# Optimization experiments

Measured on AMD Instinct MI355X. Metric: run time of the kernel, lower is better.

Reference implementation:

```python
import jax, jax.numpy as jnp
import numpy as np


def setup_inputs() -> dict:
    key = jax.random.key(0)
    ks = jax.random.split(key, 10)
    N1, N2, F, D, E = 50000, 50000, 1024, 128, 1000000
    s = 0.02
    return {
        "x_gene": jax.random.normal(ks[0], (N1, F), jnp.float32),
        "x_cell": jax.random.normal(ks[1], (N2, F), jnp.float32),
        "edge_label_index": jax.random.randint(ks[2], (2, E), 0, N1, jnp.int64 if jax.config.jax_enable_x64 else jnp.int32),
        "W1": jax.random.normal(ks[3], (F, D), jnp.float32) * s,
        "b1": jnp.zeros((D,), jnp.float32),
        "W2": jax.random.normal(ks[4], (F, D), jnp.float32) * s,
        "b2": jnp.zeros((D,), jnp.float32),
        "Wm1": jax.random.normal(ks[5], (2 * D, 64), jnp.float32) * s,
        "bm1": jnp.zeros((64,), jnp.float32),
        "Wm2": jax.random.normal(ks[6], (64, 32), jnp.float32) * s,
        "bm2": jnp.zeros((32,), jnp.float32),
        "Wm3": jax.random.normal(ks[7], (32, 1), jnp.float32) * s,
        "bm3": jnp.zeros((1,), jnp.float32),
    }


def reference(x_gene, x_cell, edge_label_index, W1, b1, W2, b2, Wm1, bm1, Wm2, bm2, Wm3, bm3):
    # Node-type linear projections (dropout is identity in eval mode)
    h1 = x_gene @ W1 + b1          # [N1, D]
    h2 = x_cell @ W2 + b2          # [N2, D]
    # Edge gather + concat
    ef = jnp.concatenate([h1[edge_label_index[0]], h2[edge_label_index[1]]], axis=-1)  # [E, 2D]
    # 3-layer MLP classifier
    h = jax.nn.relu(ef @ Wm1 + bm1)
    h = jax.nn.relu(h @ Wm2 + bm2)
    pred = (h @ Wm3 + bm3)[..., 0]  # squeeze(-1) -> [E]
    return pred
```

## Files before the change

### kernel.cpp

```cpp
#include <hip/hip_runtime.h>
#include <hip/hip_bf16.h>
#include <stdint.h>

typedef __attribute__((ext_vector_type(8))) short short8;
typedef __attribute__((ext_vector_type(4))) float float4v;

__device__ __forceinline__ float bf2f(uint16_t u) {
    union { uint32_t i; float f; } v; v.i = ((uint32_t)u) << 16; return v.f;
}
__device__ __forceinline__ uint16_t f2bf(float f) {
    union { float f; uint32_t i; } v; v.f = f;
    uint32_t x = v.i;
    uint32_t r = (x + 0x7fffu + ((x >> 16) & 1u)) >> 16;
    return (uint16_t)r;
}
__device__ __forceinline__ float relu_nanprop(float x) {
    return 0.5f * (x + fabsf(x));
}

__global__ __launch_bounds__(256) void precompute_kernel(
    const float* __restrict__ W1, const float* __restrict__ W2,
    const float* __restrict__ Wm1,
    const float* __restrict__ b1, const float* __restrict__ b2,
    const float* __restrict__ bm1,
    uint16_t* __restrict__ A1T, uint16_t* __restrict__ A2T,
    float* __restrict__ tbias)
{
    int b = blockIdx.x, t = threadIdx.x;
    if (b < 512) {
        int g   = b * 256 + t;
        int mat = g >> 16;
        int rem = g & 65535;
        int n   = rem >> 10;
        int f   = rem & 1023;
        const float* W  = mat ? W2 : W1;
        const float* wm = Wm1 + mat * 128 * 64;
        const float4* Wrow = (const float4*)(W + (size_t)f * 128);
        float acc = 0.f;
        #pragma unroll
        for (int c = 0; c < 32; ++c) {
            float4 w = Wrow[c];
            acc += w.x * wm[(c * 4 + 0) * 64 + n];
            acc += w.y * wm[(c * 4 + 1) * 64 + n];
            acc += w.z * wm[(c * 4 + 2) * 64 + n];
            acc += w.w * wm[(c * 4 + 3) * 64 + n];
        }
        (mat ? A2T : A1T)[(size_t)n * 1024 + f] = f2bf(acc);
    } else if (t < 64) {
        float acc = bm1[t];
        for (int d = 0; d < 128; ++d) acc += b1[d] * Wm1[d * 64 + t];
        for (int d = 0; d < 128; ++d) acc += b2[d] * Wm1[(128 + d) * 64 + t];
        tbias[t] = acc;
    }
}

__global__ __launch_bounds__(256) void gemm64_kernel(
    const float* __restrict__ X1, const float* __restrict__ X2,
    const uint16_t* __restrict__ A1T, const uint16_t* __restrict__ A2T,
    uint16_t* __restrict__ G1, uint16_t* __restrict__ G2, int M1, int M2)
{
    const int which = blockIdx.y;
    const float* __restrict__ X     = which ? X2  : X1;
    const uint16_t* __restrict__ BT = which ? A2T : A1T;
    uint16_t* __restrict__ G        = which ? G2  : G1;
    const int M = which ? M2 : M1;

    const int blockRow = blockIdx.x * 128;
    if (blockRow >= M) return;

    __shared__ uint16_t As[128 * 64];

    const int t    = threadIdx.x;
    const int wid  = t >> 6;
    const int lane = t & 63;
    const int m    = lane & 15;
    const int q    = lane >> 4;

    float4v acc[2][4];
    #pragma unroll
    for (int r = 0; r < 2; ++r)
        #pragma unroll
        for (int nt = 0; nt < 4; ++nt)
            acc[r][nt] = (float4v){0.f, 0.f, 0.f, 0.f};

    for (int kk = 0; kk < 16; ++kk) {
        float4 av0[4], av1[4];
        int    dstc[4];
        #pragma unroll
        for (int it = 0; it < 4; ++it) {
            int c   = it * 256 + t;
            int row = c >> 3, pc = c & 7;
            int lc  = pc ^ (row & 7);
            int grow = blockRow + row; if (grow >= M) grow = M - 1;
            const float4* src = (const float4*)(X + (size_t)grow * 1024 + kk * 64 + lc * 8);
            av0[it] = src[0];
            av1[it] = src[1];
            dstc[it] = c * 8;
        }
        __syncthreads();
        #pragma unroll
        for (int it = 0; it < 4; ++it) {
            uint4 pk;
            pk.x = (uint32_t)f2bf(av0[it].x) | ((uint32_t)f2bf(av0[it].y) << 16);
            pk.y = (uint32_t)f2bf(av0[it].z) | ((uint32_t)f2bf(av0[it].w) << 16);
            pk.z = (uint32_t)f2bf(av1[it].x) | ((uint32_t)f2bf(av1[it].y) << 16);
            pk.w = (uint32_t)f2bf(av1[it].z) | ((uint32_t)f2bf(av1[it].w) << 16);
            *(uint4*)(As + dstc[it]) = pk;
        }
        __syncthreads();

        #pragma unroll
        for (int s = 0; s < 2; ++s) {
            short8 af[2], bfr[4];
            #pragma unroll
            for (int r = 0; r < 2; ++r) {
                int row = wid * 32 + r * 16 + m;
                int pc  = (s * 4 + q) ^ (row & 7);
                af[r] = *(const short8*)(As + row * 64 + pc * 8);
            }
            #pragma unroll
            for (int nt = 0; nt < 4; ++nt) {
                int n = nt * 16 + m;
                bfr[nt] = *(const short8*)(BT + (size_t)n * 1024 + kk * 64 + (s * 4 + q) * 8);
            }
            #pragma unroll
            for (int r = 0; r < 2; ++r)
                #pragma unroll
                for (int nt = 0; nt < 4; ++nt)
                    acc[r][nt] = __builtin_amdgcn_mfma_f32_16x16x32_bf16(
                        af[r], bfr[nt], acc[r][nt], 0, 0, 0);
        }
    }

    #pragma unroll
    for (int r = 0; r < 2; ++r) {
        #pragma unroll
        for (int reg = 0; reg < 4; ++reg) {
            int grow = blockRow + wid * 32 + r * 16 + q * 4 + reg;
            if (grow < M) {
                #pragma unroll
                for (int nt = 0; nt < 4; ++nt)
                    G[(size_t)grow * 64 + nt * 16 + m] = f2bf(acc[r][nt][reg]);
            }
        }
    }
}

__global__ __launch_bounds__(256) void edge_mlp_kernel(
    const uint16_t* __restrict__ g1, const uint16_t* __restrict__ g2,
    const float* __restrict__ tbias, const int* __restrict__ eidx,
    const float* __restrict__ Wm2, const float* __restrict__ bm2,
    const float* __restrict__ Wm3, const float* __restrict__ bm3,
    float* __restrict__ out, int E)
{
    int e = blockIdx.x * 256 + threadIdx.x;
    if (e >= E) e = E - 1;
    int src = eidx[e];
    int dst = eidx[E + e];
    const uint4* r1 = (const uint4*)(g1 + (size_t)src * 64);
    const uint4* r2 = (const uint4*)(g2 + (size_t)dst * 64);

    float u[32];
    #pragma unroll
    for (int j = 0; j < 32; ++j) u[j] = bm2[j];

    #pragma unroll
    for (int c = 0; c < 8; ++c) {
        uint4 a = r1[c], b = r2[c];
        uint32_t aw[4] = { a.x, a.y, a.z, a.w };
        uint32_t bw[4] = { b.x, b.y, b.z, b.w };
        float tv[8];
        #pragma unroll
        for (int h = 0; h < 4; ++h) {
            float alo, ahi, blo, bhi;
            { union { uint32_t i; float f; } v; v.i = aw[h] << 16;        alo = v.f; }
            { union { uint32_t i; float f; } v; v.i = aw[h] & 0xffff0000u; ahi = v.f; }
            { union { uint32_t i; float f; } v; v.i = bw[h] << 16;        blo = v.f; }
            { union { uint32_t i; float f; } v; v.i = bw[h] & 0xffff0000u; bhi = v.f; }
            tv[2 * h]     = relu_nanprop(alo + blo + tbias[c * 8 + 2 * h]);
            tv[2 * h + 1] = relu_nanprop(ahi + bhi + tbias[c * 8 + 2 * h + 1]);
        }
        #pragma unroll
        for (int i = 0; i < 8; ++i) {
            const float* wrow = Wm2 + (c * 8 + i) * 32;
            #pragma unroll
            for (int j = 0; j < 32; ++j)
                u[j] = fmaf(tv[i], wrow[j], u[j]);
        }
    }

    float p = bm3[0];
    #pragma unroll
    for (int j = 0; j < 32; ++j)
        p += relu_nanprop(u[j]) * Wm3[j];
    out[e] = p;
}

extern "C" void kernel_launch(void* const* d_in, const int* in_sizes, int n_in,
                              void* d_out, int out_size, void* d_ws, size_t ws_size,
                              hipStream_t stream) {
    const float* x_gene = (const float*)d_in[0];
    const float* x_cell = (const float*)d_in[1];
    const int*   eidx   = (const int*)d_in[2];
    const float* W1  = (const float*)d_in[3];
    const float* b1  = (const float*)d_in[4];
    const float* W2  = (const float*)d_in[5];
    const float* b2  = (const float*)d_in[6];
    const float* Wm1 = (const float*)d_in[7];
    const float* bm1 = (const float*)d_in[8];
    const float* Wm2 = (const float*)d_in[9];
    const float* bm2 = (const float*)d_in[10];
    const float* Wm3 = (const float*)d_in[11];
    const float* bm3 = (const float*)d_in[12];

    const int M1 = in_sizes[0] / 1024;
    const int M2 = in_sizes[1] / 1024;
    const int E  = in_sizes[2] / 2;

    uint8_t* ws = (uint8_t*)d_ws;
    uint16_t* A1T   = (uint16_t*)(ws + 0);
    uint16_t* A2T   = (uint16_t*)(ws + 131072);
    float*    tbias = (float*)(ws + 262144);
    uint16_t* G1    = (uint16_t*)(ws + 524288);
    size_t g1_bytes = ((size_t)M1 * 64 * 2 + 127) & ~(size_t)127;
    uint16_t* G2    = (uint16_t*)(ws + 524288 + g1_bytes);

    precompute_kernel<<<513, 256, 0, stream>>>(
        W1, W2, Wm1, b1, b2, bm1, A1T, A2T, tbias);

    int Mmax = M1 > M2 ? M1 : M2;
    dim3 ggrid((Mmax + 127) / 128, 2);
    gemm64_kernel<<<ggrid, 256, 0, stream>>>(x_gene, x_cell, A1T, A2T, G1, G2, M1, M2);

    edge_mlp_kernel<<<(E + 255) / 256, 256, 0, stream>>>(
        G1, G2, tbias, eidx, Wm2, bm2, Wm3, bm3, (float*)d_out, E);
}
```

Before: 573.7 us.

## Use MFMA for edge MLP layer 2, retile GEMM, and restructure precompute

The edge MLP now writes the relu'd hidden layer as bf16 into shared memory and computes the 64x32 second layer with bf16 MFMA, then finishes layer 3 with a cross-lane shuffle reduction instead of 2048 scalar FMAs per thread. The projection GEMM moves to 64-row blocks with 128-wide K steps, doubling the grid for more parallelism. The precompute kernel is reorganised to give coalesced weight reads, and it also emits a transposed bf16 copy of Wm2. This lowers ALU work in the edge stage, at the cost of bf16 rounding of the hidden activations and extra shared memory use.

```diff
diff --git a/kernel.cpp b/kernel.cpp
--- a/kernel.cpp
+++ b/kernel.cpp
@@ -14,43 +14,41 @@
     uint32_t r = (x + 0x7fffu + ((x >> 16) & 1u)) >> 16;
     return (uint16_t)r;
 }
-__device__ __forceinline__ float relu_nanprop(float x) {
-    return 0.5f * (x + fabsf(x));
-}
 
 __global__ __launch_bounds__(256) void precompute_kernel(
     const float* __restrict__ W1, const float* __restrict__ W2,
-    const float* __restrict__ Wm1,
+    const float* __restrict__ Wm1, const float* __restrict__ Wm2,
     const float* __restrict__ b1, const float* __restrict__ b2,
     const float* __restrict__ bm1,
     uint16_t* __restrict__ A1T, uint16_t* __restrict__ A2T,
-    float* __restrict__ tbias)
+    float* __restrict__ tbias, uint16_t* __restrict__ Wm2bfT)
 {
     int b = blockIdx.x, t = threadIdx.x;
     if (b < 512) {
-        int g   = b * 256 + t;
-        int mat = g >> 16;
-        int rem = g & 65535;
-        int n   = rem >> 10;
-        int f   = rem & 1023;
-        const float* W  = mat ? W2 : W1;
-        const float* wm = Wm1 + mat * 128 * 64;
-        const float4* Wrow = (const float4*)(W + (size_t)f * 128);
+        int g   = b * 4 + (t >> 6);
+        int mat = g >> 10;
+        int f   = g & 1023;
+        int n   = t & 63;
+        const float* W    = mat ? W2 : W1;
+        const float* wm   = Wm1 + mat * 128 * 64;
+        const float* Wrow = W + (size_t)f * 128;
         float acc = 0.f;
-        #pragma unroll
-        for (int c = 0; c < 32; ++c) {
-            float4 w = Wrow[c];
-            acc += w.x * wm[(c * 4 + 0) * 64 + n];
-            acc += w.y * wm[(c * 4 + 1) * 64 + n];
-            acc += w.z * wm[(c * 4 + 2) * 64 + n];
-            acc += w.w * wm[(c * 4 + 3) * 64 + n];
-        }
+        #pragma unroll 8
+        for (int d = 0; d < 128; ++d)
+            acc = fmaf(Wrow[d], wm[d * 64 + n], acc);
         (mat ? A2T : A1T)[(size_t)n * 1024 + f] = f2bf(acc);
-    } else if (t < 64) {
-        float acc = bm1[t];
-        for (int d = 0; d < 128; ++d) acc += b1[d] * Wm1[d * 64 + t];
-        for (int d = 0; d < 128; ++d) acc += b2[d] * Wm1[(128 + d) * 64 + t];
-        tbias[t] = acc;
+    } else {
+        int n  = t >> 3;
+        int k0 = (t & 7) * 8;
+        #pragma unroll
+        for (int i = 0; i < 8; ++i)
+            Wm2bfT[n * 64 + k0 + i] = f2bf(Wm2[(size_t)(k0 + i) * 32 + n]);
+        if (t < 64) {
+            float acc = bm1[t];
+            for (int d = 0; d < 128; ++d) acc += b1[d] * Wm1[d * 64 + t];
+            for (int d = 0; d < 128; ++d) acc += b2[d] * Wm1[(128 + d) * 64 + t];
+            tbias[t] = acc;
+        }
     }
 }
 
@@ -65,10 +63,10 @@
     uint16_t* __restrict__ G        = which ? G2  : G1;
     const int M = which ? M2 : M1;
 
-    const int blockRow = blockIdx.x * 128;
+    const int blockRow = blockIdx.x * 64;
     if (blockRow >= M) return;
 
-    __shared__ uint16_t As[128 * 64];
+    __shared__ uint16_t As[64 * 128];
 
     const int t    = threadIdx.x;
     const int wid  = t >> 6;
@@ -76,23 +74,20 @@
     const int m    = lane & 15;
     const int q    = lane >> 4;
 
-    float4v acc[2][4];
-    #pragma unroll
-    for (int r = 0; r < 2; ++r)
-        #pragma unroll
-        for (int nt = 0; nt < 4; ++nt)
-            acc[r][nt] = (float4v){0.f, 0.f, 0.f, 0.f};
-
-    for (int kk = 0; kk < 16; ++kk) {
+    float4v acc[4];
+    #pragma unroll
+    for (int nt = 0; nt < 4; ++nt) acc[nt] = (float4v){0.f, 0.f, 0.f, 0.f};
+
+    for (int kk = 0; kk < 8; ++kk) {
         float4 av0[4], av1[4];
         int    dstc[4];
         #pragma unroll
         for (int it = 0; it < 4; ++it) {
             int c   = it * 256 + t;
-            int row = c >> 3, pc = c & 7;
+            int row = c >> 4, pc = c & 15;
             int lc  = pc ^ (row & 7);
             int grow = blockRow + row; if (grow >= M) grow = M - 1;
-            const float4* src = (const float4*)(X + (size_t)grow * 1024 + kk * 64 + lc * 8);
+            const float4* src = (const float4*)(X + (size_t)grow * 1024 + kk * 128 + lc * 8);
             av0[it] = src[0];
             av1[it] = src[1];
             dstc[it] = c * 8;
@@ -110,38 +105,30 @@
         __syncthreads();
 
         #pragma unroll
-        for (int s = 0; s < 2; ++s) {
-            short8 af[2], bfr[4];
-            #pragma unroll
-            for (int r = 0; r < 2; ++r) {
-                int row = wid * 32 + r * 16 + m;
-                int pc  = (s * 4 + q) ^ (row & 7);
-                af[r] = *(const short8*)(As + row * 64 + pc * 8);
-            }
+        for (int p = 0; p < 4; ++p) {
+            short8 af, bfr[4];
+            int row = wid * 16 + m;
+            int pc  = (p * 4 + q) ^ (row & 7);
+            af = *(const short8*)(As + row * 128 + pc * 8);
             #pragma unroll
             for (int nt = 0; nt < 4; ++nt) {
                 int n = nt * 16 + m;
-                bfr[nt] = *(const short8*)(BT + (size_t)n * 1024 + kk * 64 + (s * 4 + q) * 8);
+                bfr[nt] = *(const short8*)(BT + (size_t)n * 1024 + kk * 128 + (p * 4 + q) * 8);
             }
             #pragma unroll
-            for (int r = 0; r < 2; ++r)
-                #pragma unroll
-                for (int nt = 0; nt < 4; ++nt)
-                    acc[r][nt] = __builtin_amdgcn_mfma_f32_16x16x32_bf16(
-                        af[r], bfr[nt], acc[r][nt], 0, 0, 0);
-        }
-    }
-
-    #pragma unroll
-    for (int r = 0; r < 2; ++r) {
-        #pragma unroll
-        for (int reg = 0; reg < 4; ++reg) {
-            int grow = blockRow + wid * 32 + r * 16 + q * 4 + reg;
-            if (grow < M) {
-                #pragma unroll
-                for (int nt = 0; nt < 4; ++nt)
-                    G[(size_t)grow * 64 + nt * 16 + m] = f2bf(acc[r][nt][reg]);
-            }
+            for (int nt = 0; nt < 4; ++nt)
+                acc[nt] = __builtin_amdgcn_mfma_f32_16x16x32_bf16(
+                    af, bfr[nt], acc[nt], 0, 0, 0);
+        }
+    }
+
+    #pragma unroll
+    for (int reg = 0; reg < 4; ++reg) {
+        int grow = blockRow + wid * 16 + q * 4 + reg;
+        if (grow < M) {
+            #pragma unroll
+            for (int nt = 0; nt < 4; ++nt)
+                G[(size_t)grow * 64 + nt * 16 + m] = f2bf(acc[nt][reg]);
         }
     }
 }
@@ -149,27 +136,45 @@
 __global__ __launch_bounds__(256) void edge_mlp_kernel(
     const uint16_t* __restrict__ g1, const uint16_t* __restrict__ g2,
     const float* __restrict__ tbias, const int* __restrict__ eidx,
-    const float* __restrict__ Wm2, const float* __restrict__ bm2,
+    const uint16_t* __restrict__ Wm2bfT, const float* __restrict__ bm2,
     const float* __restrict__ Wm3, const float* __restrict__ bm3,
     float* __restrict__ out, int E)
 {
-    int e = blockIdx.x * 256 + threadIdx.x;
-    if (e >= E) e = E - 1;
-    int src = eidx[e];
-    int dst = eidx[E + e];
+    __shared__ uint16_t T[256 * 64];
+
+    const int t    = threadIdx.x;
+    const int wid  = t >> 6;
+    const int lane = t & 63;
+    const int m    = lane & 15;
+    const int q    = lane >> 4;
+
+    short8 bfrag[2][2];
+    #pragma unroll
+    for (int s = 0; s < 2; ++s)
+        #pragma unroll
+        for (int nt = 0; nt < 2; ++nt)
+            bfrag[s][nt] = *(const short8*)(Wm2bfT + (nt * 16 + m) * 64 + s * 32 + q * 8);
+
+    const float bm2a = bm2[m],      bm2b = bm2[16 + m];
+    const float w3a  = Wm3[m],      w3b  = Wm3[16 + m];
+    const float b3   = bm3[0];
+
+    const int tileBase = blockIdx.x * 256;
+    int e = tileBase + t; if (e >= E) e = E - 1;
+    const int src = eidx[e];
+    const int dst = eidx[E + e];
     const uint4* r1 = (const uint4*)(g1 + (size_t)src * 64);
     const uint4* r2 = (const uint4*)(g2 + (size_t)dst * 64);
 
-    float u[32];
-    #pragma unroll
-    for (int j = 0; j < 32; ++j) u[j] = bm2[j];
+    uint4 A[8], B[8];
+    #pragma unroll
+    for (int c = 0; c < 8; ++c) { A[c] = r1[c]; B[c] = r2[c]; }
 
     #pragma unroll
     for (int c = 0; c < 8; ++c) {
-        uint4 a = r1[c], b = r2[c];
-        uint32_t aw[4] = { a.x, a.y, a.z, a.w };
-        uint32_t bw[4] = { b.x, b.y, b.z, b.w };
-        float tv[8];
+        uint32_t aw[4] = { A[c].x, A[c].y, A[c].z, A[c].w };
+        uint32_t bw[4] = { B[c].x, B[c].y, B[c].z, B[c].w };
+        uint32_t pw[4];
         #pragma unroll
         for (int h = 0; h < 4; ++h) {
             float alo, ahi, blo, bhi;
@@ -177,23 +182,49 @@
             { union { uint32_t i; float f; } v; v.i = aw[h] & 0xffff0000u; ahi = v.f; }
             { union { uint32_t i; float f; } v; v.i = bw[h] << 16;        blo = v.f; }
             { union { uint32_t i; float f; } v; v.i = bw[h] & 0xffff0000u; bhi = v.f; }
-            tv[2 * h]     = relu_nanprop(alo + blo + tbias[c * 8 + 2 * h]);
-            tv[2 * h + 1] = relu_nanprop(ahi + bhi + tbias[c * 8 + 2 * h + 1]);
-        }
-        #pragma unroll
-        for (int i = 0; i < 8; ++i) {
-            const float* wrow = Wm2 + (c * 8 + i) * 32;
-            #pragma unroll
-            for (int j = 0; j < 32; ++j)
-                u[j] = fmaf(tv[i], wrow[j], u[j]);
-        }
-    }
-
-    float p = bm3[0];
-    #pragma unroll
-    for (int j = 0; j < 32; ++j)
-        p += relu_nanprop(u[j]) * Wm3[j];
-    out[e] = p;
+            float t0 = fmaxf(alo + blo + tbias[c * 8 + 2 * h],     0.f);
+            float t1 = fmaxf(ahi + bhi + tbias[c * 8 + 2 * h + 1], 0.f);
+            pw[h] = (uint32_t)f2bf(t0) | ((uint32_t)f2bf(t1) << 16);
+        }
+        uint4 pk; pk.x = pw[0]; pk.y = pw[1]; pk.z = pw[2]; pk.w = pw[3];
+        int pc = c ^ (t & 7);
+        *(uint4*)(T + t * 64 + pc * 8) = pk;
+    }
+    __syncthreads();
+
+    float4v acc[4][2];
+    #pragma unroll
+    for (int r = 0; r < 4; ++r) {
+        acc[r][0] = (float4v){0.f, 0.f, 0.f, 0.f};
+        acc[r][1] = (float4v){0.f, 0.f, 0.f, 0.f};
+    }
+    #pragma unroll
+    for (int r = 0; r < 4; ++r) {
+        const int row = wid * 64 + r * 16 + m;
+        #pragma unroll
+        for (int s = 0; s < 2; ++s) {
+            const int pc = (s * 4 + q) ^ (row & 7);
+            short8 af = *(const short8*)(T + row * 64 + pc * 8);
+            acc[r][0] = __builtin_amdgcn_mfma_f32_16x16x32_bf16(af, bfrag[s][0], acc[r][0], 0, 0, 0);
+            acc[r][1] = __builtin_amdgcn_mfma_f32_16x16x32_bf16(af, bfrag[s][1], acc[r][1], 0, 0, 0);
+        }
+    }
+
+    #pragma unroll
+    for (int r = 0; r < 4; ++r) {
+        #pragma unroll
+        for (int reg = 0; reg < 4; ++reg) {
+            float v0 = fmaxf(acc[r][0][reg] + bm2a, 0.f);
+            float v1 = fmaxf(acc[r][1][reg] + bm2b, 0.f);
+            float p  = fmaf(v0, w3a, v1 * w3b);
+            p += __shfl_xor(p, 1);
+            p += __shfl_xor(p, 2);
+            p += __shfl_xor(p, 4);
+            p += __shfl_xor(p, 8);
+            int eo = tileBase + wid * 64 + r * 16 + q * 4 + reg;
+            if (m == 0 && eo < E) out[eo] = p + b3;
+        }
+    }
 }
 
 extern "C" void kernel_launch(void* const* d_in, const int* in_sizes, int n_in,
@@ -218,20 +249,21 @@
     const int E  = in_sizes[2] / 2;
 
     uint8_t* ws = (uint8_t*)d_ws;
-    uint16_t* A1T   = (uint16_t*)(ws + 0);
-    uint16_t* A2T   = (uint16_t*)(ws + 131072);
-    float*    tbias = (float*)(ws + 262144);
-    uint16_t* G1    = (uint16_t*)(ws + 524288);
-    size_t g1_bytes = ((size_t)M1 * 64 * 2 + 127) & ~(size_t)127;
-    uint16_t* G2    = (uint16_t*)(ws + 524288 + g1_bytes);
+    uint16_t* A1T    = (uint16_t*)(ws + 0);
+    uint16_t* A2T    = (uint16_t*)(ws + 131072);
+    float*    tbias  = (float*)(ws + 262144);
+    uint16_t* Wm2bfT = (uint16_t*)(ws + 262400);
+    uint16_t* G1     = (uint16_t*)(ws + 524288);
+    size_t g1_bytes  = ((size_t)M1 * 64 * 2 + 127) & ~(size_t)127;
+    uint16_t* G2     = (uint16_t*)(ws + 524288 + g1_bytes);
 
     precompute_kernel<<<513, 256, 0, stream>>>(
-        W1, W2, Wm1, b1, b2, bm1, A1T, A2T, tbias);
+        W1, W2, Wm1, Wm2, b1, b2, bm1, A1T, A2T, tbias, Wm2bfT);
 
     int Mmax = M1 > M2 ? M1 : M2;
-    dim3 ggrid((Mmax + 127) / 128, 2);
+    dim3 ggrid((Mmax + 63) / 64, 2);
     gemm64_kernel<<<ggrid, 256, 0, stream>>>(x_gene, x_cell, A1T, A2T, G1, G2, M1, M2);
 
     edge_mlp_kernel<<<(E + 255) / 256, 256, 0, stream>>>(
-        G1, G2, tbias, eidx, Wm2, bm2, Wm3, bm3, (float*)d_out, E);
-}
+        G1, G2, tbias, eidx, Wm2bfT, bm2, Wm3, bm3, (float*)d_out, E);
+}
```

Result: faster. 543.6 us (-5.2%).
